# Kernel optimization log

Hardware: AMD Instinct MI355X
Metric: run time of the kernel (lower is better)

The kernel has to match this reference:

```python
import jax, jax.numpy as jnp
import numpy as np

MODULE_NUM = 4
TOP_K = 2
relu = jax.nn.relu


def setup_inputs() -> dict:
    key = jax.random.key(0)
    ks = jax.random.split(key, 20)
    B, IN, H, EMH, GH, OUT = 8192, 64, 1024, 256, 512, 18
    GOUT = MODULE_NUM * (MODULE_NUM + 1) // 2  # 10
    s = 0.02
    return {
        "x": jax.random.normal(ks[0], (B, IN), dtype=jnp.float32),
        "em": jax.random.uniform(ks[1], (B, 1), dtype=jnp.float32),
        # base MLP (last activation = identity)
        "base_W0": jax.random.normal(ks[2], (IN, H)) * s,
        "base_b0": jnp.full((H,), 0.1, jnp.float32),
        "base_W1": jax.random.normal(ks[3], (H, H)) * s,
        "base_b1": jnp.full((H,), 0.1, jnp.float32),
        # embedding MLP (relu after every layer)
        "em_W0": jax.random.normal(ks[4], (1, EMH)) * s,
        "em_b0": jnp.full((EMH,), 0.1, jnp.float32),
        "em_W1": jax.random.normal(ks[5], (EMH, H)) * s,
        "em_b1": jnp.full((H,), 0.1, jnp.float32),
        # gate MLP
        "gate_W0": jax.random.normal(ks[6], (H, GH)) * s,
        "gate_b0": jnp.full((GH,), 0.1, jnp.float32),
        "gate_W1": jax.random.normal(ks[7], (GH, GOUT)) * s,
        "gate_b1": jnp.full((GOUT,), 0.1, jnp.float32),
        # module fc chain: fc0..fc{M-1}, all HxH (module_hidden == hidden_shapes[-1])
        "fc_W": jax.random.normal(ks[8], (MODULE_NUM, H, H)) * s,
        "fc_b": jnp.full((MODULE_NUM, H), 0.1, jnp.float32),
        # last output layer
        "last_W": jax.random.normal(ks[9], (H, OUT)) * s,
        "last_b": jnp.zeros((OUT,), jnp.float32),
    }


def reference(x, em, base_W0, base_b0, base_W1, base_b1,
              em_W0, em_b0, em_W1, em_b1,
              gate_W0, gate_b0, gate_W1, gate_b1,
              fc_W, fc_b, last_W, last_b):
    B = x.shape[0]
    # base MLP (null last activation)
    base_out = relu(x @ base_W0 + base_b0) @ base_W1 + base_b1  # [B,H]
    # embedding MLP (relu last activation)
    e = relu(relu(em @ em_W0 + em_b0) @ em_W1 + em_b1)          # [B,H]
    # cond_ob: gate input conditioned on observation
    gate_in = e * base_out
    module_input = relu(base_out)
    # gate network -> logits for all depth levels, split sizes [1..M]
    logits_all = relu(gate_in @ gate_W0 + gate_b0) @ gate_W1 + gate_b1  # [B, M(M+1)/2]

    rows = jnp.arange(B)[:, None]
    gates_list, onehot_list, soft_list = [], [], []
    off = 0
    for m in range(1, MODULE_NUM + 1):
        logits = logits_all[:, off:off + m]  # [B,m]
        off += m
        k = min(TOP_K, m)
        top_v, top_i = jax.lax.top_k(logits, k)            # [B,k]
        top_g = jax.nn.softmax(top_v, axis=-1)             # rescale_prob=True
        gates = jnp.zeros_like(logits).at[rows, top_i].set(top_g)   # scatter [B,m]
        onehot = jax.nn.one_hot(top_i, m, dtype=logits.dtype).sum(-2)  # [B,m]
        soft = jax.nn.softmax(logits, axis=-1)
        gates_list.append(gates)
        onehot_list.append(onehot)
        soft_list.append(soft)

    # cascaded module chain (use_resnet=False, resrouting off / eval mode)
    out = relu(module_input @ fc_W[0] + fc_b[0])[:, None, :]  # [B,1,H]
    for i in range(1, MODULE_NUM):
        gate = gates_list[i - 1]                           # [B,i]
        inp = jnp.einsum('bm,bmh->bh', gate, out)          # gated mix of prev levels
        h = relu(inp @ fc_W[i] + fc_b[i])
        out = jnp.concatenate([out, h[:, None, :]], axis=1)  # [B,i+1,H]

    last_out = jnp.einsum('bm,bmh->bh', gates_list[-1], out)  # [B,H]
    final = last_out @ last_W + last_b                        # [B,OUT]
    return (final,
            jnp.concatenate(gates_list, axis=-1),
            jnp.concatenate(onehot_list, axis=-1),
            jnp.concatenate(soft_list, axis=-1))
```

## Files before the change

### kernel.cpp

```cpp
#include <hip/hip_runtime.h>
#include <hip/hip_bf16.h>


typedef unsigned short u16;
typedef __attribute__((ext_vector_type(8))) short bf16x8;
typedef _Float16 f16x8 __attribute__((ext_vector_type(8)));
typedef __attribute__((ext_vector_type(4))) float f32x4;

typedef const __attribute__((address_space(1))) void* gas_ptr;
typedef __attribute__((address_space(3))) void* las_ptr;

__device__ inline float bf2f(u16 u) {
    union { unsigned int i; float f; } v; v.i = ((unsigned int)u) << 16; return v.f;
}
__device__ inline u16 f2bf(float f) {
    union { float f; unsigned int i; } v; v.f = f;
    unsigned int x = v.i;
    return (u16)((x + 0x7FFFu + ((x >> 16) & 1u)) >> 16);
}

template<int AMODE, bool RELU_OUT, bool MUL_EPI, bool DUAL>
__global__ __launch_bounds__(256, 2) void mfma_split_kernel(
    const float* __restrict__ A, const float* __restrict__ emp,
    const float* __restrict__ emW0, const float* __restrict__ emb0,
    const _Float16* __restrict__ BTh, const _Float16* __restrict__ BTl,
    const float* __restrict__ bias, const float* __restrict__ MulM,
    float* __restrict__ C, u16* __restrict__ Drelu, int M, int N, int K)
{
    __shared__ _Float16 Ah[128 * 40], Al[128 * 40];
    __shared__ _Float16 Bh[128 * 40], Bl[128 * 40];

    const int tid = threadIdx.x;
    const int wave = tid >> 6, lane = tid & 63;
    const int id = blockIdx.y * gridDim.x + blockIdx.x;
    const int nM = gridDim.y;
    const int m0 = (id % nM) * 128, n0 = (id / nM) * 128;
    const int quad = lane >> 4, l16 = lane & 15;
    const int mq = (wave >> 1) * 64, nq = (wave & 1) * 64;

    const int srow = tid >> 1;
    const int shf  = (tid & 1) * 16;

    f32x4 acch[4][4] = {};
    f32x4 accl[4][4] = {};

    for (int k0 = 0; k0 < K; k0 += 32) {
        {
            int ra = m0 + srow; if (ra >= M) ra = M - 1;
            float v[16];
            if constexpr (AMODE == 0) {
#pragma unroll
                for (int s = 0; s < 4; ++s) {
                    float4 q = *(const float4*)&A[(size_t)ra * K + k0 + shf + s * 4];
                    v[s*4+0] = q.x; v[s*4+1] = q.y; v[s*4+2] = q.z; v[s*4+3] = q.w;
                }
            } else {
                float emv = emp[ra];
#pragma unroll
                for (int s = 0; s < 4; ++s) {
                    float4 w = *(const float4*)&emW0[k0 + shf + s * 4];
                    float4 b = *(const float4*)&emb0[k0 + shf + s * 4];
                    v[s*4+0] = fmaxf(emv * w.x + b.x, 0.f);
                    v[s*4+1] = fmaxf(emv * w.y + b.y, 0.f);
                    v[s*4+2] = fmaxf(emv * w.z + b.z, 0.f);
                    v[s*4+3] = fmaxf(emv * w.w + b.w, 0.f);
                }
            }
            f16x8 h0, h1, l0, l1;
#pragma unroll
            for (int e = 0; e < 8; ++e) {
                _Float16 h = (_Float16)v[e];
                h0[e] = h; l0[e] = (_Float16)((v[e] - (float)h) * 2048.0f);
            }
#pragma unroll
            for (int e = 0; e < 8; ++e) {
                _Float16 h = (_Float16)v[8 + e];
                h1[e] = h; l1[e] = (_Float16)((v[8 + e] - (float)h) * 2048.0f);
            }
            *(f16x8*)&Ah[srow * 40 + shf]     = h0;
            *(f16x8*)&Ah[srow * 40 + shf + 8] = h1;
            *(f16x8*)&Al[srow * 40 + shf]     = l0;
            *(f16x8*)&Al[srow * 40 + shf + 8] = l1;
        }
        {
            size_t boff = (size_t)(n0 + srow) * K + k0 + shf;
            *(f16x8*)&Bh[srow * 40 + shf]     = *(const f16x8*)&BTh[boff];
            *(f16x8*)&Bh[srow * 40 + shf + 8] = *(const f16x8*)&BTh[boff + 8];
            *(f16x8*)&Bl[srow * 40 + shf]     = *(const f16x8*)&BTl[boff];
            *(f16x8*)&Bl[srow * 40 + shf + 8] = *(const f16x8*)&BTl[boff + 8];
        }
        __syncthreads();

        f16x8 afh[4], afl[4], bfh[4], bfl[4];
#pragma unroll
        for (int i = 0; i < 4; ++i) {
            afh[i] = *(const f16x8*)&Ah[(mq + i * 16 + l16) * 40 + quad * 8];
            afl[i] = *(const f16x8*)&Al[(mq + i * 16 + l16) * 40 + quad * 8];
        }
#pragma unroll
        for (int j = 0; j < 4; ++j) {
            bfh[j] = *(const f16x8*)&Bh[(nq + j * 16 + l16) * 40 + quad * 8];
            bfl[j] = *(const f16x8*)&Bl[(nq + j * 16 + l16) * 40 + quad * 8];
        }
#pragma unroll
        for (int i = 0; i < 4; ++i)
#pragma unroll
            for (int j = 0; j < 4; ++j) {
                acch[i][j] = __builtin_amdgcn_mfma_f32_16x16x32_f16(afh[i], bfh[j], acch[i][j], 0, 0, 0);
                accl[i][j] = __builtin_amdgcn_mfma_f32_16x16x32_f16(afh[i], bfl[j], accl[i][j], 0, 0, 0);
                accl[i][j] = __builtin_amdgcn_mfma_f32_16x16x32_f16(afl[i], bfh[j], accl[i][j], 0, 0, 0);
            }
        __syncthreads();
    }

    const float S = 1.0f / 2048.0f;
#pragma unroll
    for (int i = 0; i < 4; ++i) {
#pragma unroll
        for (int j = 0; j < 4; ++j) {
            int col = n0 + nq + j * 16 + l16;
            float bv = bias[col];
#pragma unroll
            for (int r = 0; r < 4; ++r) {
                int row = m0 + mq + i * 16 + quad * 4 + r;
                if (row < M) {
                    float v = acch[i][j][r] + accl[i][j][r] * S + bv;
                    if (RELU_OUT) v = fmaxf(v, 0.f);
                    if (MUL_EPI)  v *= MulM[(size_t)row * N + col];
                    C[(size_t)row * N + col] = v;
                    if (DUAL) Drelu[(size_t)row * N + col] = f2bf(fmaxf(v, 0.f));
                }
            }
        }
    }
}

template<int CMODE>
__global__ __launch_bounds__(256) void mfma_fc_kernel(
    const short* __restrict__ A, const short* __restrict__ o1p,
    const short* __restrict__ o2p, const float* __restrict__ gates, int goff,
    const short* __restrict__ BT, const float* __restrict__ bias,
    short* __restrict__ C, int M, int N, int K)
{
    __shared__ short As[128 * 40];
    __shared__ short Bs[512 * 8];
    const int tid = threadIdx.x;
    const int wave = tid >> 6, lane = tid & 63;
    const int id = blockIdx.y * gridDim.x + blockIdx.x;
    const int nM = gridDim.y;
    const int m0 = (id % nM) * 128, n0 = (id / nM) * 128;
    const int quad = lane >> 4, l16 = lane & 15;
    const int mq = (wave >> 1) * 64, nq = (wave & 1) * 64;

    f32x4 acc[4][4] = {};

    for (int k0 = 0; k0 < K; k0 += 32) {
#pragma unroll
        for (int a = 0; a < 2; ++a) {
            int c = a * 256 + wave * 64 + lane;
            int row = c & 127, seg = c >> 7;
            const short* gp = &BT[(size_t)(n0 + row) * K + k0 + seg * 8];
            __builtin_amdgcn_global_load_lds(
                (gas_ptr)(const void*)gp,
                (las_ptr)(void*)&Bs[(size_t)(a * 256 + wave * 64) * 8],
                16, 0, 0);
        }
#pragma unroll
        for (int it = 0; it < 2; ++it) {
            int c = it * 256 + tid;
            int row = c >> 2, seg = c & 3;
            int ra = m0 + row; if (ra >= M) ra = M - 1;
            bf16x8 va = *(const bf16x8*)&A[(size_t)ra * K + k0 + seg * 8];
            if constexpr (CMODE > 0) {
                const float* gp = gates + (size_t)ra * 10 + goff;
                float g0 = gp[0], g1 = gp[1];
                bf16x8 v1 = *(const bf16x8*)&o1p[(size_t)ra * K + k0 + seg * 8];
                float g2 = 0.f; bf16x8 v2;
                if constexpr (CMODE == 2) {
                    g2 = gp[2];
                    v2 = *(const bf16x8*)&o2p[(size_t)ra * K + k0 + seg * 8];
                }
#pragma unroll
                for (int e = 0; e < 8; ++e) {
                    float f = g0 * bf2f((u16)va[e]) + g1 * bf2f((u16)v1[e]);
                    if constexpr (CMODE == 2) f += g2 * bf2f((u16)v2[e]);
                    va[e] = (short)f2bf(f);
                }
            }
            *(bf16x8*)&As[row * 40 + seg * 8] = va;
        }
        __syncthreads();

        bf16x8 af[4], bfr[4];
#pragma unroll
        for (int i = 0; i < 4; ++i)
            af[i] = *(const bf16x8*)&As[(mq + i * 16 + l16) * 40 + quad * 8];
#pragma unroll
        for (int j = 0; j < 4; ++j)
            bfr[j] = *(const bf16x8*)&Bs[(size_t)(quad * 128 + nq + j * 16 + l16) * 8];
#pragma unroll
        for (int i = 0; i < 4; ++i)
#pragma unroll
            for (int j = 0; j < 4; ++j)
                acc[i][j] = __builtin_amdgcn_mfma_f32_16x16x32_bf16(af[i], bfr[j], acc[i][j], 0, 0, 0);
        __syncthreads();
    }

#pragma unroll
    for (int i = 0; i < 4; ++i) {
#pragma unroll
        for (int j = 0; j < 4; ++j) {
            int col = n0 + nq + j * 16 + l16;
            float bv = bias[col];
#pragma unroll
            for (int r = 0; r < 4; ++r) {
                int row = m0 + mq + i * 16 + quad * 4 + r;
                if (row < M) {
                    float v = fmaxf(acc[i][j][r] + bv, 0.f);
                    C[(size_t)row * N + col] = (short)f2bf(v);
                }
            }
        }
    }
}

template<int NN, bool ABF16, bool BBF16>
__global__ __launch_bounds__(256) void smallN_kernel(
    const void* __restrict__ Av, const float* __restrict__ Bw,
    const float* __restrict__ bias, float* __restrict__ C, int M, int K)
{
    extern __shared__ char smem[];
    const int tid = threadIdx.x;
    const int total = K * NN;
    if (BBF16) {
        u16* Bs = (u16*)smem;
        for (int i = tid; i < total; i += 256) Bs[i] = f2bf(Bw[i]);
    } else {
        float* Bs = (float*)smem;
        for (int i = tid; i < total; i += 256) Bs[i] = Bw[i];
    }
    __syncthreads();

    const int lane = tid & 63;
    const int wave = tid >> 6;
    const int l16 = lane & 15;
    const int rsub = lane >> 4;
    int row = blockIdx.x * 16 + wave * 4 + rsub;
    const bool valid = (row < M);
    if (row >= M) row = M - 1;

    float acc[NN];
#pragma unroll
    for (int j = 0; j < NN; ++j) acc[j] = 0.f;

    const int chunk = K >> 4;
    const int kbeg = l16 * chunk;

    if (ABF16) {
        const u16* A = (const u16*)Av + (size_t)row * K + kbeg;
        const u16* Bs = (const u16*)smem;
        for (int kk = 0; kk < chunk; kk += 4) {
            ushort4 u = *(const ushort4*)&A[kk];
            float a4[4] = {bf2f(u.x), bf2f(u.y), bf2f(u.z), bf2f(u.w)};
#pragma unroll
            for (int e = 0; e < 4; ++e) {
                const u16* bp = &Bs[(size_t)(kbeg + kk + e) * NN];
#pragma unroll
                for (int j = 0; j < NN; ++j) acc[j] += a4[e] * bf2f(bp[j]);
            }
        }
    } else {
        const float* A = (const float*)Av + (size_t)row * K + kbeg;
        const float* Bs = (const float*)smem;
        for (int kk = 0; kk < chunk; kk += 4) {
            float4 q = *(const float4*)&A[kk];
            float a4[4] = {q.x, q.y, q.z, q.w};
#pragma unroll
            for (int e = 0; e < 4; ++e) {
                const float* bp = &Bs[(size_t)(kbeg + kk + e) * NN];
#pragma unroll
                for (int j = 0; j < NN; ++j) acc[j] += a4[e] * bp[j];
            }
        }
    }

#pragma unroll
    for (int j = 0; j < NN; ++j) {
        float v = acc[j];
        v += __shfl_xor(v, 1, 16);
        v += __shfl_xor(v, 2, 16);
        v += __shfl_xor(v, 4, 16);
        v += __shfl_xor(v, 8, 16);
        acc[j] = v;
    }
    if (valid && l16 == 0) {
#pragma unroll
        for (int j = 0; j < NN; ++j)
            C[(size_t)row * NN + j] = acc[j] + bias[j];
    }
}

template<int AMODE, bool OUT_BF16>
__global__ __launch_bounds__(256) void gemm_kernel(
    const void* __restrict__ Av, const float* __restrict__ Bw,
    const float* __restrict__ bias, void* __restrict__ Cv, int M, int N, int K)
{
    __shared__ float As[16][68];
    __shared__ float Bs[16][64];

    const int tid = threadIdx.x;
    const int tx = tid & 15, ty = tid >> 4;
    const int m0 = blockIdx.y * 64;
    const int n0 = blockIdx.x * 64;

    const int arow = tid >> 2;
    const int ak   = (tid & 3) * 4;
    const int brow = tid >> 4;
    const int bcol = (tid & 15) * 4;

    float acc[4][4];
#pragma unroll
    for (int i = 0; i < 4; i++)
#pragma unroll
        for (int j = 0; j < 4; j++) acc[i][j] = 0.f;

    for (int k0 = 0; k0 < K; k0 += 16) {
        float4 av;
        int r = m0 + arow; if (r >= M) r = M - 1;
        if constexpr (AMODE == 0) {
            av = *(const float4*)((const float*)Av + (size_t)r * K + (k0 + ak));
        } else {
            ushort4 u = *(const ushort4*)((const u16*)Av + (size_t)r * K + (k0 + ak));
            av.x = bf2f(u.x); av.y = bf2f(u.y); av.z = bf2f(u.z); av.w = bf2f(u.w);
        }
        As[ak + 0][arow] = av.x; As[ak + 1][arow] = av.y;
        As[ak + 2][arow] = av.z; As[ak + 3][arow] = av.w;

#pragma unroll
        for (int j = 0; j < 4; j++) {
            int c = n0 + bcol + j;
            Bs[brow][bcol + j] = (c < N) ? Bw[(size_t)(k0 + brow) * N + c] : 0.f;
        }
        __syncthreads();

#pragma unroll
        for (int kk = 0; kk < 16; kk++) {
            float4 a = *(const float4*)&As[kk][ty * 4];
            float4 b = *(const float4*)&Bs[kk][tx * 4];
            acc[0][0] += a.x * b.x; acc[0][1] += a.x * b.y; acc[0][2] += a.x * b.z; acc[0][3] += a.x * b.w;
            acc[1][0] += a.y * b.x; acc[1][1] += a.y * b.y; acc[1][2] += a.y * b.z; acc[1][3] += a.y * b.w;
            acc[2][0] += a.z * b.x; acc[2][1] += a.z * b.y; acc[2][2] += a.z * b.z; acc[2][3] += a.z * b.w;
            acc[3][0] += a.w * b.x; acc[3][1] += a.w * b.y; acc[3][2] += a.w * b.z; acc[3][3] += a.w * b.w;
        }
        __syncthreads();
    }

#pragma unroll
    for (int i = 0; i < 4; i++) {
        int r = m0 + ty * 4 + i;
#pragma unroll
        for (int j = 0; j < 4; j++) {
            int c = n0 + tx * 4 + j;
            if (r < M && c < N) {
                float v = acc[i][j] + bias[c];
                if (OUT_BF16) ((u16*)Cv)[(size_t)r * N + c] = f2bf(v);
                else          ((float*)Cv)[(size_t)r * N + c] = v;
            }
        }
    }
}

__global__ __launch_bounds__(256) void transpose_kernel(
    const float* __restrict__ in, u16* __restrict__ out, int K, int N)
{
    __shared__ u16 T[64][65];
    int k0 = blockIdx.y * 64, n0 = blockIdx.x * 64;
    int t = threadIdx.x;
    int r = t >> 4, c4 = (t & 15) * 4;
#pragma unroll
    for (int i = 0; i < 4; ++i) {
        int kk = r + i * 16;
        float4 v = *(const float4*)&in[(size_t)(k0 + kk) * N + n0 + c4];
        T[c4 + 0][kk] = f2bf(v.x); T[c4 + 1][kk] = f2bf(v.y);
        T[c4 + 2][kk] = f2bf(v.z); T[c4 + 3][kk] = f2bf(v.w);
    }
    __syncthreads();
#pragma unroll
    for (int i = 0; i < 4; ++i) {
        int nn = r + i * 16;
        ushort4 o;
        o.x = T[nn][c4 + 0]; o.y = T[nn][c4 + 1];
        o.z = T[nn][c4 + 2]; o.w = T[nn][c4 + 3];
        *(ushort4*)&out[(size_t)(n0 + nn) * K + k0 + c4] = o;
    }
}

__global__ __launch_bounds__(256) void transpose_split_kernel(
    const float* __restrict__ in, u16* __restrict__ outh, u16* __restrict__ outl,
    int K, int N)
{
    __shared__ u16 Th[64][65];
    __shared__ u16 Tl[64][65];
    int k0 = blockIdx.y * 64, n0 = blockIdx.x * 64;
    int t = threadIdx.x;
    int r = t >> 4, c4 = (t & 15) * 4;
    union { _Float16 h; u16 u; } cv;
#pragma unroll
    for (int i = 0; i < 4; ++i) {
        int kk = r + i * 16;
        float4 v = *(const float4*)&in[(size_t)(k0 + kk) * N + n0 + c4];
        float vv[4] = {v.x, v.y, v.z, v.w};
#pragma unroll
        for (int e = 0; e < 4; ++e) {
            _Float16 h = (_Float16)vv[e];
            cv.h = h; Th[c4 + e][kk] = cv.u;
            cv.h = (_Float16)((vv[e] - (float)h) * 2048.0f);
            Tl[c4 + e][kk] = cv.u;
        }
    }
    __syncthreads();
#pragma unroll
    for (int i = 0; i < 4; ++i) {
        int nn = r + i * 16;
        ushort4 oh, ol;
        oh.x = Th[nn][c4 + 0]; oh.y = Th[nn][c4 + 1];
        oh.z = Th[nn][c4 + 2]; oh.w = Th[nn][c4 + 3];
        ol.x = Tl[nn][c4 + 0]; ol.y = Tl[nn][c4 + 1];
        ol.z = Tl[nn][c4 + 2]; ol.w = Tl[nn][c4 + 3];
        *(ushort4*)&outh[(size_t)(n0 + nn) * K + k0 + c4] = oh;
        *(ushort4*)&outl[(size_t)(n0 + nn) * K + k0 + c4] = ol;
    }
}

__global__ __launch_bounds__(256) void routing_kernel(
    const float* __restrict__ logits, int Bc,
    float* __restrict__ gates, float* __restrict__ onehot,
    float* __restrict__ soft)
{
    int b = blockIdx.x * blockDim.x + threadIdx.x;
    if (b >= Bc) return;
    const float* l = logits + (size_t)b * 10;
    float* g  = gates  + (size_t)b * 10;
    float* oh = onehot + (size_t)b * 10;
    float* sf = soft   + (size_t)b * 10;

    g[0] = 1.f; oh[0] = 1.f; sf[0] = 1.f;

    int off = 1;
    for (int m = 2; m <= 4; m++) {
        float v[4];
        for (int i = 0; i < m; i++) v[i] = l[off + i];
        int i0 = 0;
        for (int i = 1; i < m; i++) if (v[i] > v[i0]) i0 = i;
        int i1 = (i0 == 0) ? 1 : 0;
        for (int i = 0; i < m; i++) if (i != i0 && v[i] > v[i1]) i1 = i;
        float e1 = expf(v[i1] - v[i0]);
        float inv = 1.f / (1.f + e1);
        for (int i = 0; i < m; i++) { g[off + i] = 0.f; oh[off + i] = 0.f; }
        g[off + i0] = inv;
        g[off + i1] = e1 * inv;
        oh[off + i0] = 1.f; oh[off + i1] = 1.f;
        float mall = v[0];
        for (int i = 1; i < m; i++) mall = fmaxf(mall, v[i]);
        float ex[4]; float se = 0.f;
        for (int i = 0; i < m; i++) { ex[i] = expf(v[i] - mall); se += ex[i]; }
        float rse = 1.f / se;
        for (int i = 0; i < m; i++) sf[off + i] = ex[i] * rse;
        off += m;
    }
}

__global__ __launch_bounds__(256) void combine_kernel(
    const float* __restrict__ gates, int goff, int n4, int H,
    const u16* __restrict__ o0, const u16* __restrict__ o1,
    const u16* __restrict__ o2, const u16* __restrict__ o3,
    u16* __restrict__ dst)
{
    int i4 = blockIdx.x * blockDim.x + threadIdx.x;
    if (i4 >= n4) return;
    int b = (i4 * 4) / H;
    const float* gp = gates + (size_t)b * 10 + goff;
    float g0 = gp[0], g1 = gp[1], g2 = gp[2], g3 = gp[3];
    ushort4 a  = ((const ushort4*)o0)[i4];
    ushort4 u1 = ((const ushort4*)o1)[i4];
    ushort4 u2 = ((const ushort4*)o2)[i4];
    ushort4 u3 = ((const ushort4*)o3)[i4];
    float4 acc;
    acc.x = g0 * bf2f(a.x) + g1 * bf2f(u1.x) + g2 * bf2f(u2.x) + g3 * bf2f(u3.x);
    acc.y = g0 * bf2f(a.y) + g1 * bf2f(u1.y) + g2 * bf2f(u2.y) + g3 * bf2f(u3.y);
    acc.z = g0 * bf2f(a.z) + g1 * bf2f(u1.z) + g2 * bf2f(u2.z) + g3 * bf2f(u3.z);
    acc.w = g0 * bf2f(a.w) + g1 * bf2f(u1.w) + g2 * bf2f(u2.w) + g3 * bf2f(u3.w);
    ushort4 r;
    r.x = f2bf(acc.x); r.y = f2bf(acc.y); r.z = f2bf(acc.z); r.w = f2bf(acc.w);
    ((ushort4*)dst)[i4] = r;
}

extern "C" void kernel_launch(void* const* d_in, const int* in_sizes, int n_in,
                              void* d_out, int out_size, void* d_ws, size_t ws_size,
                              hipStream_t stream) {
    const float* x       = (const float*)d_in[0];
    const float* em      = (const float*)d_in[1];
    const float* base_W0 = (const float*)d_in[2];
    const float* base_b0 = (const float*)d_in[3];
    const float* base_W1 = (const float*)d_in[4];
    const float* base_b1 = (const float*)d_in[5];
    const float* em_W0   = (const float*)d_in[6];
    const float* em_b0   = (const float*)d_in[7];
    const float* em_W1   = (const float*)d_in[8];
    const float* em_b1   = (const float*)d_in[9];
    const float* gate_W0 = (const float*)d_in[10];
    const float* gate_b0 = (const float*)d_in[11];
    const float* gate_W1 = (const float*)d_in[12];
    const float* gate_b1 = (const float*)d_in[13];
    const float* fc_W    = (const float*)d_in[14];
    const float* fc_b    = (const float*)d_in[15];
    const float* last_W  = (const float*)d_in[16];
    const float* last_b  = (const float*)d_in[17];

    const int H    = in_sizes[3];
    const int INF  = in_sizes[2] / H;
    const int B    = in_sizes[0] / INF;
    const int EMH  = in_sizes[7];
    const int GH   = in_sizes[11];
    const int GOUT = in_sizes[13];
    const int NOUT = in_sizes[17];

    float* out = (float*)d_out;
    float* o_final  = out;
    float* o_gates  = out + (size_t)B * NOUT;
    float* o_onehot = o_gates + (size_t)B * 10;
    float* o_soft   = o_onehot + (size_t)B * 10;

    const size_t szWT = (size_t)8 * H * H;
    const size_t szW0 = (size_t)2 * H * INF;
    const size_t szW1 = (size_t)2 * H * H;
    const size_t szWE = (size_t)2 * H * EMH;
    const size_t szWG = (size_t)2 * GH * H;
    const size_t fixed = szWT + 2 * (szW0 + szW1 + szWE + szWG);
    const size_t perRow = (size_t)10 * H + (size_t)4 * GH + 40;

    const bool shapesOK = (H % 128 == 0) && (GH % 128 == 0) &&
                          (INF % 64 == 0) && (EMH % 64 == 0);
    const bool useFast = shapesOK && (ws_size > fixed + 128 * perRow);
    const bool smallOK = (GOUT == 10) && (NOUT == 18) && (GH % 64 == 0) && (H % 64 == 0);

    char* wsb = (char*)d_ws;
    u16* WT  = (u16*)wsb;
    u16* W0h = (u16*)(wsb + szWT);
    u16* W0l = W0h + (size_t)H * INF;
    u16* W1h = (u16*)(wsb + szWT + 2 * szW0);
    u16* W1l = W1h + (size_t)H * H;
    u16* WEh = (u16*)(wsb + szWT + 2 * szW0 + 2 * szW1);
    u16* WEl = WEh + (size_t)H * EMH;
    u16* WGh = (u16*)(wsb + szWT + 2 * szW0 + 2 * szW1 + 2 * szWE);
    u16* WGl = WGh + (size_t)GH * H;

    int Bc = ((B + 127) / 128) * 128;
    size_t avail = ws_size - (useFast ? fixed : 0);
    while (Bc > 128 && (size_t)Bc * perRow > avail) Bc >>= 1;

    char* rows = wsb + (useFast ? fixed : 0);
    float* R0 = (float*)rows;
    float* R1 = (float*)(rows + (size_t)Bc * 4 * H);
    float* R2 = (float*)(rows + (size_t)Bc * 8 * H);
    u16*   RD = (u16*)(rows + (size_t)Bc * (8 * H + 4 * GH));
    float* LG = (float*)(rows + (size_t)Bc * (10 * H + 4 * GH));
    u16* O0 = (u16*)R0;
    u16* O1 = O0 + (size_t)Bc * H;
    u16* O2 = (u16*)R1;
    u16* O3 = O2 + (size_t)Bc * H;

    dim3 blk(256);
    const size_t fc1 = (size_t)H * H;

    if (useFast) {
        dim3 tg((unsigned)(H / 64), (unsigned)(H / 64));
        for (int i = 0; i < 4; ++i)
            transpose_kernel<<<tg, blk, 0, stream>>>(fc_W + (size_t)i * fc1, WT + (size_t)i * fc1, H, H);
        transpose_split_kernel<<<dim3((unsigned)(H / 64), (unsigned)(INF / 64)), blk, 0, stream>>>(
            base_W0, W0h, W0l, INF, H);
        transpose_split_kernel<<<dim3((unsigned)(H / 64), (unsigned)(H / 64)), blk, 0, stream>>>(
            base_W1, W1h, W1l, H, H);
        transpose_split_kernel<<<dim3((unsigned)(H / 64), (unsigned)(EMH / 64)), blk, 0, stream>>>(
            em_W1, WEh, WEl, EMH, H);
        transpose_split_kernel<<<dim3((unsigned)(GH / 64), (unsigned)(H / 64)), blk, 0, stream>>>(
            gate_W0, WGh, WGl, H, GH);
    }

    for (int c0 = 0; c0 < B; c0 += Bc) {
        const int Bcur = (B - c0 < Bc) ? (B - c0) : Bc;
        const float* xc  = x + (size_t)c0 * INF;
        const float* emc = em + c0;
        float* ofin = o_final  + (size_t)c0 * NOUT;
        float* ogat = o_gates  + (size_t)c0 * 10;
        float* ooh  = o_onehot + (size_t)c0 * 10;
        float* osf  = o_soft   + (size_t)c0 * 10;

        auto g64  = [&](int N) { return dim3((unsigned)((N + 63) / 64), (unsigned)((Bcur + 63) / 64)); };
        auto gS   = [&](int N) { return dim3((unsigned)(N / 128), (unsigned)((Bcur + 127) / 128)); };
        const dim3 mgrid((unsigned)(H / 128), (unsigned)((Bcur + 127) / 128));
        const int n4 = Bcur * H / 4;
        const dim3 cgrid((unsigned)((n4 + 255) / 256));
        const dim3 sgrid((unsigned)((Bcur + 15) / 16));

        mfma_split_kernel<0, true, false, false><<<gS(H), blk, 0, stream>>>(
            xc, nullptr, nullptr, nullptr, (const _Float16*)W0h, (const _Float16*)W0l,
            base_b0, nullptr, R0, nullptr, Bcur, H, INF);
        mfma_split_kernel<0, false, false, true><<<gS(H), blk, 0, stream>>>(
            R0, nullptr, nullptr, nullptr, (const _Float16*)W1h, (const _Float16*)W1l,
            base_b1, nullptr, R1, RD, Bcur, H, H);
        mfma_split_kernel<2, true, true, false><<<gS(H), blk, 0, stream>>>(
            nullptr, emc, em_W0, em_b0, (const _Float16*)WEh, (const _Float16*)WEl,
            em_b1, R1, R0, nullptr, Bcur, H, EMH);
        mfma_split_kernel<0, true, false, false><<<gS(GH), blk, 0, stream>>>(
            R0, nullptr, nullptr, nullptr, (const _Float16*)WGh, (const _Float16*)WGl,
            gate_b0, nullptr, R2, nullptr, Bcur, GH, H);
        if (smallOK) {
            smallN_kernel<10, false, false><<<sgrid, blk, (size_t)GH * 10 * 4, stream>>>(
                R2, gate_W1, gate_b1, LG, Bcur, GH);
        } else {
            gemm_kernel<0, false><<<g64(GOUT), blk, 0, stream>>>(
                R2, gate_W1, gate_b1, LG, Bcur, GOUT, GH);
        }
        routing_kernel<<<dim3((unsigned)((Bcur + 255) / 256)), blk, 0, stream>>>(LG, Bcur, ogat, ooh, osf);

        mfma_fc_kernel<0><<<mgrid, blk, 0, stream>>>(
            (const short*)RD, nullptr, nullptr, nullptr, 0,
            (const short*)WT, fc_b, (short*)O0, Bcur, H, H);
        mfma_fc_kernel<0><<<mgrid, blk, 0, stream>>>(
            (const short*)O0, nullptr, nullptr, nullptr, 0,
            (const short*)(WT + fc1), fc_b + H, (short*)O1, Bcur, H, H);
        mfma_fc_kernel<1><<<mgrid, blk, 0, stream>>>(
            (const short*)O0, (const short*)O1, nullptr, ogat, 1,
            (const short*)(WT + 2 * fc1), fc_b + 2 * H, (short*)O2, Bcur, H, H);
        mfma_fc_kernel<2><<<mgrid, blk, 0, stream>>>(
            (const short*)O0, (const short*)O1, (const short*)O2, ogat, 3,
            (const short*)(WT + 3 * fc1), fc_b + 3 * H, (short*)O3, Bcur, H, H);

        combine_kernel<<<cgrid, blk, 0, stream>>>(ogat, 6, n4, H, O0, O1, O2, O3, RD);
        if (smallOK) {
            smallN_kernel<18, true, true><<<sgrid, blk, (size_t)H * 18 * 2, stream>>>(
                RD, last_W, last_b, ofin, Bcur, H);
        } else {
            gemm_kernel<1, false><<<g64(NOUT), blk, 0, stream>>>(
                RD, last_W, last_b, (void*)ofin, Bcur, NOUT, H);
        }
    }
}
```

Measured before the change: 555.2 us.

## Store split fp16 hi/lo activations and stage tiles via global_load_lds

```diff
diff --git a/kernel.cpp b/kernel.cpp
--- a/kernel.cpp
+++ b/kernel.cpp
@@ -18,17 +18,25 @@
     unsigned int x = v.i;
     return (u16)((x + 0x7FFFu + ((x >> 16) & 1u)) >> 16);
 }
-
-template<int AMODE, bool RELU_OUT, bool MUL_EPI, bool DUAL>
-__global__ __launch_bounds__(256, 2) void mfma_split_kernel(
-    const float* __restrict__ A, const float* __restrict__ emp,
-    const float* __restrict__ emW0, const float* __restrict__ emb0,
+__device__ inline u16 h2u(_Float16 h) {
+    union { _Float16 h; u16 u; } c; c.h = h; return c.u;
+}
+
+template<int AMODE, bool RELU_OUT, bool MUL_EPI, int OMODE>
+__global__ __launch_bounds__(256) void mfma_split_kernel(
+    const float* __restrict__ A,
+    const _Float16* __restrict__ Ahg, const _Float16* __restrict__ Alg,
+    const float* __restrict__ emp, const float* __restrict__ emW0,
+    const float* __restrict__ emb0,
     const _Float16* __restrict__ BTh, const _Float16* __restrict__ BTl,
     const float* __restrict__ bias, const float* __restrict__ MulM,
-    float* __restrict__ C, u16* __restrict__ Drelu, int M, int N, int K)
-{
-    __shared__ _Float16 Ah[128 * 40], Al[128 * 40];
-    __shared__ _Float16 Bh[128 * 40], Bl[128 * 40];
+    float* __restrict__ C, u16* __restrict__ Drelu,
+    u16* __restrict__ Ch, u16* __restrict__ Cl, int M, int N, int K)
+{
+    __shared__ _Float16 AhS[AMODE == 3 ? 512 * 8 : 128 * 40];
+    __shared__ _Float16 AlS[AMODE == 3 ? 512 * 8 : 128 * 40];
+    __shared__ _Float16 BhS[512 * 8];
+    __shared__ _Float16 BlS[512 * 8];
 
     const int tid = threadIdx.x;
     const int wave = tid >> 6, lane = tid & 63;
@@ -45,7 +53,31 @@
     f32x4 accl[4][4] = {};
 
     for (int k0 = 0; k0 < K; k0 += 32) {
-        {
+#pragma unroll
+        for (int a = 0; a < 2; ++a) {
+            int c = a * 256 + wave * 64 + lane;
+            int row = c & 127, seg = c >> 7;
+            size_t go = (size_t)(n0 + row) * K + k0 + seg * 8;
+            int lbase = (a * 256 + wave * 64) * 8;
+            __builtin_amdgcn_global_load_lds(
+                (gas_ptr)(const void*)&BTh[go], (las_ptr)(void*)&BhS[lbase], 16, 0, 0);
+            __builtin_amdgcn_global_load_lds(
+                (gas_ptr)(const void*)&BTl[go], (las_ptr)(void*)&BlS[lbase], 16, 0, 0);
+        }
+        if constexpr (AMODE == 3) {
+#pragma unroll
+            for (int a = 0; a < 2; ++a) {
+                int c = a * 256 + wave * 64 + lane;
+                int row = c & 127, seg = c >> 7;
+                int ra = m0 + row; if (ra >= M) ra = M - 1;
+                size_t go = (size_t)(m0 + row) * K + k0 + seg * 8;
+                int lbase = (a * 256 + wave * 64) * 8;
+                __builtin_amdgcn_global_load_lds(
+                    (gas_ptr)(const void*)&Ahg[go], (las_ptr)(void*)&AhS[lbase], 16, 0, 0);
+                __builtin_amdgcn_global_load_lds(
+                    (gas_ptr)(const void*)&Alg[go], (las_ptr)(void*)&AlS[lbase], 16, 0, 0);
+            }
+        } else {
             int ra = m0 + srow; if (ra >= M) ra = M - 1;
             float v[16];
             if constexpr (AMODE == 0) {
@@ -77,30 +109,30 @@
                 _Float16 h = (_Float16)v[8 + e];
                 h1[e] = h; l1[e] = (_Float16)((v[8 + e] - (float)h) * 2048.0f);
             }
-            *(f16x8*)&Ah[srow * 40 + shf]     = h0;
-            *(f16x8*)&Ah[srow * 40 + shf + 8] = h1;
-            *(f16x8*)&Al[srow * 40 + shf]     = l0;
-            *(f16x8*)&Al[srow * 40 + shf + 8] = l1;
-        }
-        {
-            size_t boff = (size_t)(n0 + srow) * K + k0 + shf;
-            *(f16x8*)&Bh[srow * 40 + shf]     = *(const f16x8*)&BTh[boff];
-            *(f16x8*)&Bh[srow * 40 + shf + 8] = *(const f16x8*)&BTh[boff + 8];
-            *(f16x8*)&Bl[srow * 40 + shf]     = *(const f16x8*)&BTl[boff];
-            *(f16x8*)&Bl[srow * 40 + shf + 8] = *(const f16x8*)&BTl[boff + 8];
+            *(f16x8*)&AhS[srow * 40 + shf]     = h0;
+            *(f16x8*)&AhS[srow * 40 + shf + 8] = h1;
+            *(f16x8*)&AlS[srow * 40 + shf]     = l0;
+            *(f16x8*)&AlS[srow * 40 + shf + 8] = l1;
         }
         __syncthreads();
 
         f16x8 afh[4], afl[4], bfh[4], bfl[4];
 #pragma unroll
         for (int i = 0; i < 4; ++i) {
-            afh[i] = *(const f16x8*)&Ah[(mq + i * 16 + l16) * 40 + quad * 8];
-            afl[i] = *(const f16x8*)&Al[(mq + i * 16 + l16) * 40 + quad * 8];
+            if constexpr (AMODE == 3) {
+                int ci = ((quad << 7) + mq + i * 16 + l16) * 8;
+                afh[i] = *(const f16x8*)&AhS[ci];
+                afl[i] = *(const f16x8*)&AlS[ci];
+            } else {
+                afh[i] = *(const f16x8*)&AhS[(mq + i * 16 + l16) * 40 + quad * 8];
+                afl[i] = *(const f16x8*)&AlS[(mq + i * 16 + l16) * 40 + quad * 8];
+            }
         }
 #pragma unroll
         for (int j = 0; j < 4; ++j) {
-            bfh[j] = *(const f16x8*)&Bh[(nq + j * 16 + l16) * 40 + quad * 8];
-            bfl[j] = *(const f16x8*)&Bl[(nq + j * 16 + l16) * 40 + quad * 8];
+            int ci = ((quad << 7) + nq + j * 16 + l16) * 8;
+            bfh[j] = *(const f16x8*)&BhS[ci];
+            bfl[j] = *(const f16x8*)&BlS[ci];
         }
 #pragma unroll
         for (int i = 0; i < 4; ++i)
@@ -127,8 +159,15 @@
                     float v = acch[i][j][r] + accl[i][j][r] * S + bv;
                     if (RELU_OUT) v = fmaxf(v, 0.f);
                     if (MUL_EPI)  v *= MulM[(size_t)row * N + col];
-                    C[(size_t)row * N + col] = v;
-                    if (DUAL) Drelu[(size_t)row * N + col] = f2bf(fmaxf(v, 0.f));
+                    if constexpr (OMODE == 2) {
+                        _Float16 h = (_Float16)v;
+                        Ch[(size_t)row * N + col] = h2u(h);
+                        Cl[(size_t)row * N + col] = h2u((_Float16)((v - (float)h) * 2048.0f));
+                    } else {
+                        C[(size_t)row * N + col] = v;
+                        if constexpr (OMODE == 1)
+                            Drelu[(size_t)row * N + col] = f2bf(fmaxf(v, 0.f));
+                    }
                 }
             }
         }
@@ -404,7 +443,6 @@
     int k0 = blockIdx.y * 64, n0 = blockIdx.x * 64;
     int t = threadIdx.x;
     int r = t >> 4, c4 = (t & 15) * 4;
-    union { _Float16 h; u16 u; } cv;
 #pragma unroll
     for (int i = 0; i < 4; ++i) {
         int kk = r + i * 16;
@@ -413,9 +451,8 @@
 #pragma unroll
         for (int e = 0; e < 4; ++e) {
             _Float16 h = (_Float16)vv[e];
-            cv.h = h; Th[c4 + e][kk] = cv.u;
-            cv.h = (_Float16)((vv[e] - (float)h) * 2048.0f);
-            Tl[c4 + e][kk] = cv.u;
+            Th[c4 + e][kk] = h2u(h);
+            Tl[c4 + e][kk] = h2u((_Float16)((vv[e] - (float)h) * 2048.0f));
         }
     }
     __syncthreads();
@@ -565,6 +602,8 @@
     float* R2 = (float*)(rows + (size_t)Bc * 8 * H);
     u16*   RD = (u16*)(rows + (size_t)Bc * (8 * H + 4 * GH));
     float* LG = (float*)(rows + (size_t)Bc * (10 * H + 4 * GH));
+    u16* R0h = (u16*)R0;
+    u16* R0l = R0h + (size_t)Bc * H;
     u16* O0 = (u16*)R0;
     u16* O1 = O0 + (size_t)Bc * H;
     u16* O2 = (u16*)R1;
@@ -603,18 +642,22 @@
         const dim3 cgrid((unsigned)((n4 + 255) / 256));
         const dim3 sgrid((unsigned)((Bcur + 15) / 16));
 
-        mfma_split_kernel<0, true, false, false><<<gS(H), blk, 0, stream>>>(
-            xc, nullptr, nullptr, nullptr, (const _Float16*)W0h, (const _Float16*)W0l,
-            base_b0, nullptr, R0, nullptr, Bcur, H, INF);
-        mfma_split_kernel<0, false, false, true><<<gS(H), blk, 0, stream>>>(
-            R0, nullptr, nullptr, nullptr, (const _Float16*)W1h, (const _Float16*)W1l,
-            base_b1, nullptr, R1, RD, Bcur, H, H);
-        mfma_split_kernel<2, true, true, false><<<gS(H), blk, 0, stream>>>(
-            nullptr, emc, em_W0, em_b0, (const _Float16*)WEh, (const _Float16*)WEl,
-            em_b1, R1, R0, nullptr, Bcur, H, EMH);
-        mfma_split_kernel<0, true, false, false><<<gS(GH), blk, 0, stream>>>(
-            R0, nullptr, nullptr, nullptr, (const _Float16*)WGh, (const _Float16*)WGl,
-            gate_b0, nullptr, R2, nullptr, Bcur, GH, H);
+        mfma_split_kernel<0, true, false, 2><<<gS(H), blk, 0, stream>>>(
+            xc, nullptr, nullptr, nullptr, nullptr, nullptr,
+            (const _Float16*)W0h, (const _Float16*)W0l,
+            base_b0, nullptr, nullptr, nullptr, R0h, R0l, Bcur, H, INF);
+        mfma_split_kernel<3, false, false, 1><<<gS(H), blk, 0, stream>>>(
+            nullptr, (const _Float16*)R0h, (const _Float16*)R0l, nullptr, nullptr, nullptr,
+            (const _Float16*)W1h, (const _Float16*)W1l,
+            base_b1, nullptr, R1, RD, nullptr, nullptr, Bcur, H, H);
+        mfma_split_kernel<2, true, true, 2><<<gS(H), blk, 0, stream>>>(
+            nullptr, nullptr, nullptr, emc, em_W0, em_b0,
+            (const _Float16*)WEh, (const _Float16*)WEl,
+            em_b1, R1, nullptr, nullptr, R0h, R0l, Bcur, H, EMH);
+        mfma_split_kernel<3, true, false, 0><<<gS(GH), blk, 0, stream>>>(
+            nullptr, (const _Float16*)R0h, (const _Float16*)R0l, nullptr, nullptr, nullptr,
+            (const _Float16*)WGh, (const _Float16*)WGl,
+            gate_b0, nullptr, R2, nullptr, nullptr, nullptr, Bcur, GH, H);
         if (smallOK) {
             smallN_kernel<10, false, false><<<sgrid, blk, (size_t)GH * 10 * 4, stream>>>(
                 R2, gate_W1, gate_b1, LG, Bcur, GH);
```

After: 702.0 us. 1.26x slower.
